# Optimization experiments

Measured on AMD Instinct MI355X. Metric: run time of the kernel, lower is better.

The kernel has to match this reference:

```python
import jax, jax.numpy as jnp
import numpy as np

N_NODES = 100000
F_IN = 128
F_HID = 64  # gcn_filters = [64, 64]
MLP_HID = 128


def setup_inputs() -> dict:
    key = jax.random.key(0)
    ks = jax.random.split(key, 12)
    E, Q = 3200000, 1000000
    feature = jax.random.normal(ks[0], (N_NODES, F_IN), dtype=jnp.float32)
    edges = jax.random.randint(ks[1], (2, E), 0, N_NODES, dtype=jnp.int32)
    i = jax.random.randint(ks[2], (Q,), 0, N_NODES, dtype=jnp.int32)
    j = jax.random.randint(ks[3], (Q,), 0, N_NODES, dtype=jnp.int32)
    s = lambda d: 1.0 / jnp.sqrt(d)
    W1 = jax.random.normal(ks[4], (F_IN, F_HID), dtype=jnp.float32) * s(F_IN)
    b1 = jnp.zeros((F_HID,), dtype=jnp.float32)
    W2 = jax.random.normal(ks[5], (F_HID, F_HID), dtype=jnp.float32) * s(F_HID)
    b2 = jnp.zeros((F_HID,), dtype=jnp.float32)
    fc1_W = jax.random.normal(ks[6], (2 * F_HID, MLP_HID), dtype=jnp.float32) * s(2 * F_HID)
    fc1_b = jnp.zeros((MLP_HID,), dtype=jnp.float32)
    fc2_W = jax.random.normal(ks[7], (MLP_HID, 2), dtype=jnp.float32) * s(MLP_HID)
    fc2_b = jnp.zeros((2,), dtype=jnp.float32)
    return {"feature": feature, "edges": edges, "i": i, "j": j,
            "W1": W1, "b1": b1, "W2": W2, "b2": b2,
            "fc1_W": fc1_W, "fc1_b": fc1_b, "fc2_W": fc2_W, "fc2_b": fc2_b}


def _gcn_layer(x, W, b, src, dst, norm, n):
    h = x @ W
    msg = h[src] * norm[:, None]
    return jax.ops.segment_sum(msg, dst, num_segments=n) + b


def reference(feature, edges, i, j, W1, b1, W2, b2, fc1_W, fc1_b, fc2_W, fc2_b):
    n = feature.shape[0]
    loops = jnp.arange(n, dtype=edges.dtype)
    src = jnp.concatenate([edges[0], loops])
    dst = jnp.concatenate([edges[1], loops])
    deg = jax.ops.segment_sum(jnp.ones(src.shape[0], feature.dtype), dst, num_segments=n)
    dinv = jax.lax.rsqrt(jnp.maximum(deg, 1e-12))
    norm = dinv[src] * dinv[dst]
    h = jax.nn.relu(_gcn_layer(feature, W1, b1, src, dst, norm, n))
    out = _gcn_layer(h, W2, b2, src, dst, norm, n)  # [N, F_HID]
    embd = jnp.concatenate([out[i], out[j]], axis=-1)  # [Q, 2*F_HID]
    hid = jax.nn.relu(embd @ fc1_W + fc1_b)
    return hid @ fc2_W + fc2_b
```

## Files before the change

### kernel.cpp

```cpp
#include <hip/hip_runtime.h>
#include <hip/hip_bf16.h>
#include <hip/hip_fp16.h>
#include <cstdint>

#define F_IN 128
#define F_HID 64
#define NB 64
#define MAXB 2048
#define NWG 256
#define PREPB 16
#define STAGE 12800

typedef _Float16 half8 __attribute__((ext_vector_type(8)));
typedef float floatx4 __attribute__((ext_vector_type(4)));

__device__ __forceinline__ float bf2f(unsigned short u) {
  return __uint_as_float(((unsigned int)u) << 16);
}
__device__ __forceinline__ unsigned short f2bf(float f) {
  unsigned int u = __float_as_uint(f);
  u += 0x7FFFu + ((u >> 16) & 1u);
  return (unsigned short)(u >> 16);
}
__device__ __forceinline__ float h2f(unsigned short u) {
  return __half2float(__ushort_as_half(u));
}
__device__ __forceinline__ unsigned short f2h(float f) {
  return __half_as_ushort(__float2half(f));
}

__global__ __launch_bounds__(64) void k_detect(const unsigned int* __restrict__ Xw,
                                               int* __restrict__ flag) {
  int lane = threadIdx.x;
  int cnt = 0;
  for (int t = lane; t < 256; t += 64) {
    unsigned int ex = (Xw[t] >> 7) & 0xFFu;
    cnt += (ex >= 117u && ex <= 137u) ? 1 : 0;
  }
#pragma unroll
  for (int off = 32; off > 0; off >>= 1) cnt += __shfl_xor(cnt, off, 64);
  if (lane == 0) *flag = (cnt >= 128) ? 1 : 0;
}

__global__ __launch_bounds__(256) void k_front(const void* __restrict__ Xv,
                                               unsigned short* __restrict__ Xh, int total8,
                                               const void* __restrict__ W1v,
                                               const void* __restrict__ W2v,
                                               const void* __restrict__ fc1Wv,
                                               unsigned short* __restrict__ fW1,
                                               unsigned short* __restrict__ fW2,
                                               unsigned short* __restrict__ fPR,
                                               const int* __restrict__ dst,
                                               int* __restrict__ hist, int E, int B, int chunk,
                                               const int* __restrict__ flagp) {
  __shared__ int lh[MAXB];
  const int bid = blockIdx.x;
  if (bid < NWG) {
    int w = bid, tid = threadIdx.x;
    for (int b = tid; b < B; b += 256) lh[b] = 0;
    __syncthreads();
    int e0 = w * chunk, e1 = min(E, e0 + chunk);
    for (int e = e0 + tid; e < e1; e += 256) atomicAdd(&lh[dst[e] >> 6], 1);
    __syncthreads();
    for (int b = tid; b < B; b += 256) hist[w * B + b] = lh[b];
    return;
  }
  const bool isb = (*flagp != 0);
  if (bid < NWG + PREPB) {
    int tid = (bid - NWG) * 256 + threadIdx.x;
    int stride = PREPB * 256;
    for (int e = tid; e < F_IN * F_HID; e += stride) {
      int k = e >> 6, n = e & 63;
      unsigned short v = isb ? f2h(bf2f(((const unsigned short*)W1v)[e]))
                             : f2h(((const float*)W1v)[e]);
      int c = k >> 5, q = (k >> 3) & 3, j = k & 7, t = n >> 4, m = n & 15;
      fW1[((c * 4 + t) * 64 + q * 16 + m) * 8 + j] = v;
    }
    for (int e = tid; e < F_HID * F_HID; e += stride) {
      int k = e >> 6, n = e & 63;
      unsigned short v = isb ? f2h(bf2f(((const unsigned short*)W2v)[e]))
                             : f2h(((const float*)W2v)[e]);
      int c = k >> 5, q = (k >> 3) & 3, j = k & 7, t = n >> 4, m = n & 15;
      fW2[((c * 4 + t) * 64 + q * 16 + m) * 8 + j] = v;
    }
    for (int ge = tid; ge < 4 * F_HID * 64; ge += stride) {
      int g = ge >> 12, e = ge & 4095;
      int k = e >> 6, n = e & 63;
      int src = (((g & 2) ? 64 : 0) + k) * 128 + (g & 1) * 64 + n;
      unsigned short v = isb ? f2h(bf2f(((const unsigned short*)fc1Wv)[src]))
                             : f2h(((const float*)fc1Wv)[src]);
      int c = k >> 5, q = (k >> 3) & 3, j = k & 7, t = n >> 4, m = n & 15;
      fPR[g * 4096 + ((c * 4 + t) * 64 + q * 16 + m) * 8 + j] = v;
    }
    return;
  }
  int t = (bid - (NWG + PREPB)) * 256 + threadIdx.x;
  int stride = (gridDim.x - (NWG + PREPB)) * 256;
  for (; t < total8; t += stride) {
    unsigned short r[8];
    if (isb) {
      uint4 d = reinterpret_cast<const uint4*>(Xv)[t];
      r[0] = f2h(__uint_as_float(d.x << 16));
      r[1] = f2h(__uint_as_float(d.x & 0xFFFF0000u));
      r[2] = f2h(__uint_as_float(d.y << 16));
      r[3] = f2h(__uint_as_float(d.y & 0xFFFF0000u));
      r[4] = f2h(__uint_as_float(d.z << 16));
      r[5] = f2h(__uint_as_float(d.z & 0xFFFF0000u));
      r[6] = f2h(__uint_as_float(d.w << 16));
      r[7] = f2h(__uint_as_float(d.w & 0xFFFF0000u));
    } else {
      float4 a = reinterpret_cast<const float4*>(Xv)[2 * t];
      float4 b = reinterpret_cast<const float4*>(Xv)[2 * t + 1];
      r[0] = f2h(a.x); r[1] = f2h(a.y); r[2] = f2h(a.z); r[3] = f2h(a.w);
      r[4] = f2h(b.x); r[5] = f2h(b.y); r[6] = f2h(b.z); r[7] = f2h(b.w);
    }
    uint4 o;
    o.x = (unsigned int)r[0] | ((unsigned int)r[1] << 16);
    o.y = (unsigned int)r[2] | ((unsigned int)r[3] << 16);
    o.z = (unsigned int)r[4] | ((unsigned int)r[5] << 16);
    o.w = (unsigned int)r[6] | ((unsigned int)r[7] << 16);
    reinterpret_cast<uint4*>(Xh)[t] = o;
  }
}

__global__ __launch_bounds__(256) void k_bscan1(int* __restrict__ hist,
                                                int* __restrict__ btot, int B) {
  const int WPL = NWG / 64;
  int b = (blockIdx.x * 256 + threadIdx.x) >> 6;
  int lane = threadIdx.x & 63;
  if (b >= B) return;
  int v[WPL];
  int s = 0;
#pragma unroll
  for (int k = 0; k < WPL; k++) {
    v[k] = hist[(size_t)(lane * WPL + k) * B + b];
    s += v[k];
  }
  int pre = s;
#pragma unroll
  for (int off = 1; off < 64; off <<= 1) {
    int t = __shfl_up(pre, off, 64);
    if (lane >= off) pre += t;
  }
  int running = pre - s;
#pragma unroll
  for (int k = 0; k < WPL; k++) {
    int val = v[k];
    hist[(size_t)(lane * WPL + k) * B + b] = running;
    running += val;
  }
  if (lane == 63) btot[b] = running;
}

__global__ __launch_bounds__(256) void k_bscan2(const int* __restrict__ btot,
                                                int* __restrict__ boff, int B, int E) {
  __shared__ int partial[256];
  int t = threadIdx.x;
  int CH = (B + 255) / 256;
  int b0 = t * CH, b1 = min(B, b0 + CH);
  int tt = 0;
  for (int b = b0; b < b1; b++) tt += btot[b];
  partial[t] = tt;
  __syncthreads();
  if (t == 0) {
    int acc = 0;
    for (int i = 0; i < 256; i++) { int v = partial[i]; partial[i] = acc; acc += v; }
  }
  __syncthreads();
  int off = partial[t];
  for (int b = b0; b < b1; b++) { boff[b] = off; off += btot[b]; }
  if (t == 255) boff[B] = E;
}

__global__ __launch_bounds__(256) void k_bfill(const int* __restrict__ src,
                                               const int* __restrict__ dst,
                                               const int* __restrict__ hist,
                                               const int* __restrict__ boff,
                                               int* __restrict__ buck,
                                               int E, int B, int chunk) {
  __shared__ int gcur[MAXB];
  __shared__ int lexcl[MAXB];
  __shared__ int lcur[MAXB];
  __shared__ int stage[STAGE];
  __shared__ unsigned short bdex[STAGE];
  __shared__ int part[256];
  const int w = blockIdx.x, tid = threadIdx.x;
  for (int b = tid; b < B; b += 256) gcur[b] = boff[b] + hist[w * B + b];
  int e0 = w * chunk, e1 = min(E, e0 + chunk);
  for (int s0 = e0; s0 < e1; s0 += STAGE) {
    int s1 = min(e1, s0 + STAGE);
    int cnt = s1 - s0;
    for (int b = tid; b < B; b += 256) lexcl[b] = 0;
    __syncthreads();
    for (int e = s0 + tid; e < s1; e += 256) atomicAdd(&lexcl[dst[e] >> 6], 1);
    __syncthreads();
    int CH = (B + 255) >> 8;
    int b0 = tid * CH, b1 = min(B, b0 + CH);
    int s = 0;
    for (int b = b0; b < b1; b++) s += lexcl[b];
    part[tid] = s;
    __syncthreads();
    if (tid == 0) {
      int acc = 0;
      for (int i = 0; i < 256; i++) { int v = part[i]; part[i] = acc; acc += v; }
    }
    __syncthreads();
    int run = part[tid];
    for (int b = b0; b < b1; b++) {
      int v = lexcl[b];
      lexcl[b] = run;
      lcur[b] = run;
      run += v;
    }
    __syncthreads();
    for (int e = s0 + tid; e < s1; e += 256) {
      int d = dst[e];
      int b = d >> 6;
      int p = atomicAdd(&lcur[b], 1);
      stage[p] = ((d & 63) << 17) | src[e];
      bdex[p] = (unsigned short)b;
    }
    __syncthreads();
    for (int p = tid; p < cnt; p += 256) {
      int b = bdex[p];
      buck[gcur[b] + (p - lexcl[b])] = stage[p];
    }
    __syncthreads();
    for (int b = tid; b < B; b += 256) gcur[b] += lcur[b] - lexcl[b];
    __syncthreads();
  }
}

__global__ __launch_bounds__(256) void k_bsort(const int* __restrict__ buck,
                                               const int* __restrict__ boff,
                                               int* __restrict__ csr,
                                               int* __restrict__ noff,
                                               float* __restrict__ dinv, int N) {
  __shared__ int bin[NB][4];
  __shared__ int excl[NB];
  int b = blockIdx.x, tid = threadIdx.x;
  const int rep = tid & 3;
  for (int i = tid; i < NB * 4; i += 256) ((int*)bin)[i] = 0;
  __syncthreads();
  int r0 = boff[b], r1 = boff[b + 1];
  for (int r = r0 + tid; r < r1; r += 256) atomicAdd(&bin[buck[r] >> 17][rep], 1);
  __syncthreads();
  if (tid < NB)
    excl[tid] = bin[tid][0] + bin[tid][1] + bin[tid][2] + bin[tid][3];
  __syncthreads();
  if (tid == 0) {
    int acc = 0;
    for (int i = 0; i < NB; i++) { int v = excl[i]; excl[i] = acc; acc += v; }
  }
  __syncthreads();
  if (tid < NB) {
    int n = b * NB + tid;
    int c0 = bin[tid][0], c1 = bin[tid][1], c2 = bin[tid][2], c3 = bin[tid][3];
    if (n < N) {
      dinv[n] = rsqrtf((float)(c0 + c1 + c2 + c3) + 1.0f);
      noff[n] = r0 + excl[tid];
    }
    int base = excl[tid];
    bin[tid][0] = base;
    bin[tid][1] = base + c0;
    bin[tid][2] = base + c0 + c1;
    bin[tid][3] = base + c0 + c1 + c2;
  }
  if (b == gridDim.x - 1 && tid == 128) noff[N] = r1;
  __syncthreads();
  for (int r = r0 + tid; r < r1; r += 256) {
    int rec = buck[r];
    int p = atomicAdd(&bin[rec >> 17][rep], 1);
    csr[r0 + p] = rec & 0x1FFFF;
  }
}


__global__ __launch_bounds__(256, 4) void k_gemm1(const unsigned short* __restrict__ Xh,
                                                  const unsigned short* __restrict__ fW1,
                                                  const float* __restrict__ dinv,
                                                  unsigned short* __restrict__ G, int N) {
  int tid = threadIdx.x;
  const int lane = tid & 63, wave = tid >> 6;
  const int m = lane & 15, q = lane >> 4;
  half8 bfrag[4][4];
#pragma unroll
  for (int c = 0; c < 4; c++)
#pragma unroll
    for (int t = 0; t < 4; t++)
      bfrag[c][t] = *reinterpret_cast<const half8*>(fW1 + ((c * 4 + t) * 64 + lane) * 8);
  int ntiles = (N + 15) >> 4;
  for (int tile = blockIdx.x * 4 + wave; tile < ntiles; tile += gridDim.x * 4) {
    int r0 = tile << 4;
    int rm = r0 + m; rm = rm < N ? rm : N - 1;
    floatx4 acc[4] = {{0.f,0.f,0.f,0.f},{0.f,0.f,0.f,0.f},{0.f,0.f,0.f,0.f},{0.f,0.f,0.f,0.f}};
#pragma unroll
    for (int c = 0; c < 4; c++) {
      half8 a = *reinterpret_cast<const half8*>(Xh + (size_t)rm * F_IN + c * 32 + q * 8);
#pragma unroll
      for (int t = 0; t < 4; t++)
        acc[t] = __builtin_amdgcn_mfma_f32_16x16x32_f16(a, bfrag[c][t], acc[t], 0, 0, 0);
    }
#pragma unroll
    for (int rr = 0; rr < 4; rr++) {
      int grow = r0 + q * 4 + rr;
      if (grow < N) {
        float dv = dinv[grow];
#pragma unroll
        for (int t = 0; t < 4; t++)
          G[(size_t)grow * F_HID + t * 16 + m] = f2h(acc[t][rr] * dv);
      }
    }
  }
}

__global__ __launch_bounds__(256, 4) void k_gemm2(const unsigned short* __restrict__ O,
                                                  const unsigned short* __restrict__ fW2,
                                                  const float* __restrict__ dinv,
                                                  unsigned short* __restrict__ G, int N) {
  int tid = threadIdx.x;
  const int lane = tid & 63, wave = tid >> 6;
  const int m = lane & 15, q = lane >> 4;
  half8 bfrag[2][4];
#pragma unroll
  for (int c = 0; c < 2; c++)
#pragma unroll
    for (int t = 0; t < 4; t++)
      bfrag[c][t] = *reinterpret_cast<const half8*>(fW2 + ((c * 4 + t) * 64 + lane) * 8);
  int ntiles = (N + 15) >> 4;
  for (int tile = blockIdx.x * 4 + wave; tile < ntiles; tile += gridDim.x * 4) {
    int r0 = tile << 4;
    int rm = r0 + m; rm = rm < N ? rm : N - 1;
    floatx4 acc[4] = {{0.f,0.f,0.f,0.f},{0.f,0.f,0.f,0.f},{0.f,0.f,0.f,0.f},{0.f,0.f,0.f,0.f}};
#pragma unroll
    for (int c = 0; c < 2; c++) {
      half8 a = *reinterpret_cast<const half8*>(O + (size_t)rm * F_HID + c * 32 + q * 8);
#pragma unroll
      for (int t = 0; t < 4; t++)
        acc[t] = __builtin_amdgcn_mfma_f32_16x16x32_f16(a, bfrag[c][t], acc[t], 0, 0, 0);
    }
#pragma unroll
    for (int rr = 0; rr < 4; rr++) {
      int grow = r0 + q * 4 + rr;
      if (grow < N) {
        float dv = dinv[grow];
#pragma unroll
        for (int t = 0; t < 4; t++)
          G[(size_t)grow * F_HID + t * 16 + m] = f2h(acc[t][rr] * dv);
      }
    }
  }
}

template <bool RELU>
__global__ __launch_bounds__(256) void k_agg(const int* __restrict__ csr,
                                             const int* __restrict__ noff,
                                             const unsigned short* __restrict__ H,
                                             const float* __restrict__ dinv,
                                             const void* __restrict__ bias,
                                             unsigned short* __restrict__ OUT, int N,
                                             const int* __restrict__ flagp) {
  const bool isb = (*flagp != 0);
  const int lane = threadIdx.x & 63;
  const int g = lane >> 4, l16 = lane & 15;
  const int gw = (blockIdx.x * 256 + threadIdx.x) >> 6;
  const int nW = (gridDim.x * 256) >> 6;
  float bv[4];
#pragma unroll
  for (int d = 0; d < 4; d++)
    bv[d] = isb ? bf2f(((const unsigned short*)bias)[l16 * 4 + d])
                : ((const float*)bias)[l16 * 4 + d];
  for (int n = gw; n < N; n += nW) {
    int start = noff[n], end = noff[n + 1];
    float a0 = 0.f, a1 = 0.f, a2 = 0.f, a3 = 0.f;
    for (int e0 = start; e0 < end; e0 += 64) {
      int ee = e0 + lane;
      int idx = (ee < end) ? csr[ee] : 0;
      int m = end - e0; m = m < 64 ? m : 64;
      int nc = m >> 2;
      int c = 0;
      for (; c + 8 <= nc; c += 8) {
        int s[8];
#pragma unroll
        for (int u = 0; u < 8; u++) s[u] = __shfl(idx, (c + u) * 4 + g, 64);
        ushort4 v[8];
#pragma unroll
        for (int u = 0; u < 8; u++)
          v[u] = *reinterpret_cast<const ushort4*>(H + (size_t)s[u] * F_HID + l16 * 4);
#pragma unroll
        for (int u = 0; u < 8; u++) {
          a0 += h2f(v[u].x); a1 += h2f(v[u].y);
          a2 += h2f(v[u].z); a3 += h2f(v[u].w);
        }
      }
      for (; c < nc; c++) {
        int s0 = __shfl(idx, c * 4 + g, 64);
        ushort4 v0 = *reinterpret_cast<const ushort4*>(H + (size_t)s0 * F_HID + l16 * 4);
        a0 += h2f(v0.x); a1 += h2f(v0.y); a2 += h2f(v0.z); a3 += h2f(v0.w);
      }
      int rem = m & 3;
      if (rem) {
        int s0 = __shfl(idx, nc * 4 + g, 64);
        if (g < rem) {
          ushort4 v0 = *reinterpret_cast<const ushort4*>(H + (size_t)s0 * F_HID + l16 * 4);
          a0 += h2f(v0.x); a1 += h2f(v0.y); a2 += h2f(v0.z); a3 += h2f(v0.w);
        }
      }
    }
    a0 += __shfl_xor(a0, 16, 64); a0 += __shfl_xor(a0, 32, 64);
    a1 += __shfl_xor(a1, 16, 64); a1 += __shfl_xor(a1, 32, 64);
    a2 += __shfl_xor(a2, 16, 64); a2 += __shfl_xor(a2, 32, 64);
    a3 += __shfl_xor(a3, 16, 64); a3 += __shfl_xor(a3, 32, 64);
    ushort4 sv = *reinterpret_cast<const ushort4*>(H + (size_t)n * F_HID + l16 * 4);
    float dv = dinv[n];
    float o0 = (a0 + h2f(sv.x)) * dv + bv[0];
    float o1 = (a1 + h2f(sv.y)) * dv + bv[1];
    float o2 = (a2 + h2f(sv.z)) * dv + bv[2];
    float o3 = (a3 + h2f(sv.w)) * dv + bv[3];
    if (RELU) {
      o0 = fmaxf(o0, 0.f); o1 = fmaxf(o1, 0.f);
      o2 = fmaxf(o2, 0.f); o3 = fmaxf(o3, 0.f);
    }
    if (lane < 16) {
      ushort4 ov;
      ov.x = f2h(o0); ov.y = f2h(o1); ov.z = f2h(o2); ov.w = f2h(o3);
      *reinterpret_cast<ushort4*>(OUT + (size_t)n * F_HID + l16 * 4) = ov;
    }
  }
}

__global__ __launch_bounds__(512) void k_query(const unsigned short* __restrict__ O,
                                               const unsigned short* __restrict__ fPR,
                                               const int* __restrict__ qi,
                                               const int* __restrict__ qj,
                                               const void* __restrict__ fc1b,
                                               const void* __restrict__ fc2W,
                                               const void* __restrict__ fc2b,
                                               void* __restrict__ out, int Q,
                                               const int* __restrict__ flagp) {
  __shared__ unsigned short sB[4 * 4096];
  const bool isb = (*flagp != 0);
  int tid = threadIdx.x;
  {
    const uint4* srcp = reinterpret_cast<const uint4*>(fPR);
    uint4* dstp = reinterpret_cast<uint4*>(sB);
#pragma unroll
    for (int r = 0; r < 4; r++) dstp[tid + r * 512] = srcp[tid + r * 512];
  }
  const int lane = tid & 63, wave = tid >> 6;
  const int m_ = lane & 15, qk = lane >> 4;
  float bb[8], w0[8], w1[8];
#pragma unroll
  for (int T = 0; T < 8; T++) {
    int h = T * 16 + m_;
    if (isb) {
      bb[T] = bf2f(((const unsigned short*)fc1b)[h]);
      w0[T] = bf2f(((const unsigned short*)fc2W)[h * 2 + 0]);
      w1[T] = bf2f(((const unsigned short*)fc2W)[h * 2 + 1]);
    } else {
      bb[T] = ((const float*)fc1b)[h];
      w0[T] = ((const float*)fc2W)[h * 2 + 0];
      w1[T] = ((const float*)fc2W)[h * 2 + 1];
    }
  }
  float ob0 = isb ? bf2f(((const unsigned short*)fc2b)[0]) : ((const float*)fc2b)[0];
  float ob1 = isb ? bf2f(((const unsigned short*)fc2b)[1]) : ((const float*)fc2b)[1];
  __syncthreads();
  const half8* sBv = reinterpret_cast<const half8*>(sB);

  const int ntiles = (Q + 15) >> 4;
  const int nW = gridDim.x * 8;
  int tile = blockIdx.x * 8 + wave;
  if (tile >= ntiles) return;

  auto ldidx = [&](int t, int& iq, int& jq) {
    if (t < ntiles) {
      int q = t * 16 + m_;
      int qq = q < Q ? q : Q - 1;
      iq = qi[qq];
      jq = qj[qq];
    }
  };
  auto gather = [&](int iq, int jq, half8& I0, half8& I1, half8& J0, half8& J1) {
    const half8* pI = reinterpret_cast<const half8*>(O + (size_t)iq * F_HID) + qk;
    const half8* pJ = reinterpret_cast<const half8*>(O + (size_t)jq * F_HID) + qk;
    I0 = pI[0]; I1 = pI[4];
    J0 = pJ[0]; J1 = pJ[4];
  };

  int iqn = 0, jqn = 0;
  ldidx(tile, iqn, jqn);
  half8 I0, I1, J0, J1;
  gather(iqn, jqn, I0, I1, J0, J1);
  ldidx(tile + nW, iqn, jqn);

  for (; tile < ntiles; tile += nW) {
    half8 nI0, nI1, nJ0, nJ1;
    gather(iqn, jqn, nI0, nI1, nJ0, nJ1);
    ldidx(tile + 2 * nW, iqn, jqn);

    float r0[4] = {0.f, 0.f, 0.f, 0.f};
    float r1[4] = {0.f, 0.f, 0.f, 0.f};
    const floatx4 zz = {0.f, 0.f, 0.f, 0.f};
#pragma unroll
    for (int h = 0; h < 2; h++) {
      floatx4 acc[4];
#pragma unroll
      for (int tt = 0; tt < 4; tt++) acc[tt] = zz;
      __builtin_amdgcn_s_setprio(1);
#pragma unroll
      for (int tt = 0; tt < 4; tt++) {
        acc[tt] = __builtin_amdgcn_mfma_f32_16x16x32_f16(
            I0, sBv[h * 512 + tt * 64 + lane], acc[tt], 0, 0, 0);
        acc[tt] = __builtin_amdgcn_mfma_f32_16x16x32_f16(
            I1, sBv[h * 512 + (4 + tt) * 64 + lane], acc[tt], 0, 0, 0);
        acc[tt] = __builtin_amdgcn_mfma_f32_16x16x32_f16(
            J0, sBv[(2 + h) * 512 + tt * 64 + lane], acc[tt], 0, 0, 0);
        acc[tt] = __builtin_amdgcn_mfma_f32_16x16x32_f16(
            J1, sBv[(2 + h) * 512 + (4 + tt) * 64 + lane], acc[tt], 0, 0, 0);
      }
      __builtin_amdgcn_s_setprio(0);
#pragma unroll
      for (int tt = 0; tt < 4; tt++) {
        int T = h * 4 + tt;
#pragma unroll
        for (int rr = 0; rr < 4; rr++) {
          float hv = fmaxf(acc[tt][rr] + bb[T], 0.f);
          r0[rr] += hv * w0[T];
          r1[rr] += hv * w1[T];
        }
      }
      __builtin_amdgcn_sched_barrier(0);
    }
#pragma unroll
    for (int rr = 0; rr < 4; rr++) {
      float a0 = r0[rr], a1 = r1[rr];
#pragma unroll
      for (int off = 8; off > 0; off >>= 1) {
        a0 += __shfl_xor(a0, off, 16);
        a1 += __shfl_xor(a1, off, 16);
      }
      if (m_ == 0) {
        int q = tile * 16 + qk * 4 + rr;
        if (q < Q) {
          if (isb) {
            *reinterpret_cast<ushort2*>((unsigned short*)out + (size_t)q * 2) =
                make_ushort2(f2bf(a0 + ob0), f2bf(a1 + ob1));
          } else {
            *reinterpret_cast<float2*>((float*)out + (size_t)q * 2) =
                make_float2(a0 + ob0, a1 + ob1);
          }
        }
      }
    }
    I0 = nI0; I1 = nI1; J0 = nJ0; J1 = nJ1;
  }
}

extern "C" void kernel_launch(void* const* d_in, const int* in_sizes, int n_in,
                              void* d_out, int out_size, void* d_ws, size_t ws_size,
                              hipStream_t stream) {
  const void* X    = d_in[0];
  const int*  edges= (const int*)d_in[1];
  const int*  qi   = (const int*)d_in[2];
  const int*  qj   = (const int*)d_in[3];
  const void* W1   = d_in[4];
  const void* b1   = d_in[5];
  const void* W2   = d_in[6];
  const void* b2   = d_in[7];
  const void* fc1W = d_in[8];
  const void* fc1b = d_in[9];
  const void* fc2W = d_in[10];
  const void* fc2b = d_in[11];

  const int N = in_sizes[0] / F_IN;
  const int E = in_sizes[1] / 2;
  const int Q = in_sizes[2];
  const int B = (N + NB - 1) / NB;
  const int chunk = (E + NWG - 1) / NWG;

  char* ws = (char*)d_ws;
  size_t off = 0;
  auto alloc = [&](size_t bytes) -> void* {
    void* p = ws + off;
    off += (bytes + 255) & ~(size_t)255;
    return p;
  };
  int*            flag = (int*)alloc(4);
  float*          dinv = (float*)alloc((size_t)N * 4);
  unsigned short* Xh   = (unsigned short*)alloc((size_t)N * F_IN * 2);
  unsigned short* G    = (unsigned short*)alloc((size_t)N * F_HID * 2);
  unsigned short* O    = (unsigned short*)alloc((size_t)N * F_HID * 2);
  unsigned short* fW1  = (unsigned short*)alloc((size_t)F_IN * F_HID * 2);
  unsigned short* fW2  = (unsigned short*)alloc((size_t)F_HID * F_HID * 2);
  unsigned short* fPR  = (unsigned short*)alloc((size_t)4 * F_HID * 64 * 2);
  int* hist = (int*)alloc((size_t)NWG * B * 4);
  int* btot = (int*)alloc((size_t)(B + 1) * 4);
  int* boff = (int*)alloc((size_t)(B + 1) * 4);
  int* buck = (int*)alloc((size_t)E * 4);
  int* csr  = (int*)alloc((size_t)E * 4);
  int* noff = (int*)alloc((size_t)(N + 1) * 4);
  (void)ws_size; (void)n_in; (void)out_size;

  const int* esrc = edges;
  const int* edst = edges + E;

  k_detect<<<1, 64, 0, stream>>>((const unsigned int*)X, flag);
  k_front<<<2048, 256, 0, stream>>>(X, Xh, N * F_IN / 8, W1, W2, fc1W, fW1, fW2, fPR,
                                    edst, hist, E, B, chunk, flag);

  k_bscan1<<<(B + 3) / 4, 256, 0, stream>>>(hist, btot, B);
  k_bscan2<<<1, 256, 0, stream>>>(btot, boff, B, E);
  k_bfill<<<NWG, 256, 0, stream>>>(esrc, edst, hist, boff, buck, E, B, chunk);
  k_bsort<<<B, 256, 0, stream>>>(buck, boff, csr, noff, dinv, N);

  k_gemm1<<<2048, 256, 0, stream>>>(Xh, fW1, dinv, G, N);
  k_agg<true><<<2048, 256, 0, stream>>>(csr, noff, G, dinv, b1, O, N, flag);

  k_gemm2<<<2048, 256, 0, stream>>>(O, fW2, dinv, G, N);
  k_agg<false><<<2048, 256, 0, stream>>>(csr, noff, G, dinv, b2, O, N, flag);

  k_query<<<1024, 512, 0, stream>>>(O, fPR, qi, qj, fc1b, fc2W, fc2b, d_out, Q, flag);
}
```

Baseline: 438.3 us.

## Remove detect and bscan2 launches by inlining dtype detection and offset scan

Drops the separate dtype-detect kernel: each consuming kernel now scans the first 256 input words itself to decide bf16 vs fp32. Folds the single-block bucket-offset scan into k_bfill, where every block recomputes the exclusive scan of btot and block 0 writes boff. Also widens the k_bsort per-bin atomic replication from 4 to 8 to reduce shared-atomic contention. Together these remove two serial launches at the cost of redundant per-thread and per-block work.

```diff
diff --git a/kernel.cpp b/kernel.cpp
--- a/kernel.cpp
+++ b/kernel.cpp
@@ -29,17 +29,15 @@
   return __half_as_ushort(__float2half(f));
 }
 
-__global__ __launch_bounds__(64) void k_detect(const unsigned int* __restrict__ Xw,
-                                               int* __restrict__ flag) {
-  int lane = threadIdx.x;
+__device__ __forceinline__ bool detect_bf16(const void* Xv) {
+  const unsigned int* Xw = (const unsigned int*)Xv;
   int cnt = 0;
-  for (int t = lane; t < 256; t += 64) {
+#pragma unroll 8
+  for (int t = 0; t < 256; t++) {
     unsigned int ex = (Xw[t] >> 7) & 0xFFu;
     cnt += (ex >= 117u && ex <= 137u) ? 1 : 0;
   }
-#pragma unroll
-  for (int off = 32; off > 0; off >>= 1) cnt += __shfl_xor(cnt, off, 64);
-  if (lane == 0) *flag = (cnt >= 128) ? 1 : 0;
+  return cnt >= 128;
 }
 
 __global__ __launch_bounds__(256) void k_front(const void* __restrict__ Xv,
@@ -51,8 +49,7 @@
                                                unsigned short* __restrict__ fW2,
                                                unsigned short* __restrict__ fPR,
                                                const int* __restrict__ dst,
-                                               int* __restrict__ hist, int E, int B, int chunk,
-                                               const int* __restrict__ flagp) {
+                                               int* __restrict__ hist, int E, int B, int chunk) {
   __shared__ int lh[MAXB];
   const int bid = blockIdx.x;
   if (bid < NWG) {
@@ -65,7 +62,7 @@
     for (int b = tid; b < B; b += 256) hist[w * B + b] = lh[b];
     return;
   }
-  const bool isb = (*flagp != 0);
+  const bool isb = detect_bf16(Xv);
   if (bid < NWG + PREPB) {
     int tid = (bid - NWG) * 256 + threadIdx.x;
     int stride = PREPB * 256;
@@ -152,30 +149,11 @@
   if (lane == 63) btot[b] = running;
 }
 
-__global__ __launch_bounds__(256) void k_bscan2(const int* __restrict__ btot,
-                                                int* __restrict__ boff, int B, int E) {
-  __shared__ int partial[256];
-  int t = threadIdx.x;
-  int CH = (B + 255) / 256;
-  int b0 = t * CH, b1 = min(B, b0 + CH);
-  int tt = 0;
-  for (int b = b0; b < b1; b++) tt += btot[b];
-  partial[t] = tt;
-  __syncthreads();
-  if (t == 0) {
-    int acc = 0;
-    for (int i = 0; i < 256; i++) { int v = partial[i]; partial[i] = acc; acc += v; }
-  }
-  __syncthreads();
-  int off = partial[t];
-  for (int b = b0; b < b1; b++) { boff[b] = off; off += btot[b]; }
-  if (t == 255) boff[B] = E;
-}
-
 __global__ __launch_bounds__(256) void k_bfill(const int* __restrict__ src,
                                                const int* __restrict__ dst,
                                                const int* __restrict__ hist,
-                                               const int* __restrict__ boff,
+                                               const int* __restrict__ btot,
+                                               int* __restrict__ boff,
                                                int* __restrict__ buck,
                                                int E, int B, int chunk) {
   __shared__ int gcur[MAXB];
@@ -185,7 +163,28 @@
   __shared__ unsigned short bdex[STAGE];
   __shared__ int part[256];
   const int w = blockIdx.x, tid = threadIdx.x;
-  for (int b = tid; b < B; b += 256) gcur[b] = boff[b] + hist[w * B + b];
+  {
+    int CH = (B + 255) >> 8;
+    int b0 = tid * CH, b1 = min(B, b0 + CH);
+    int s = 0;
+    for (int b = b0; b < b1; b++) s += btot[b];
+    part[tid] = s;
+    __syncthreads();
+    if (tid == 0) {
+      int acc = 0;
+      for (int i = 0; i < 256; i++) { int v = part[i]; part[i] = acc; acc += v; }
+    }
+    __syncthreads();
+    int run = part[tid];
+    for (int b = b0; b < b1; b++) { lexcl[b] = run; run += btot[b]; }
+    __syncthreads();
+    for (int b = tid; b < B; b += 256) gcur[b] = lexcl[b] + hist[w * B + b];
+    if (w == 0) {
+      for (int b = tid; b < B; b += 256) boff[b] = lexcl[b];
+      if (tid == 0) boff[B] = E;
+    }
+    __syncthreads();
+  }
   int e0 = w * chunk, e1 = min(E, e0 + chunk);
   for (int s0 = e0; s0 < e1; s0 += STAGE) {
     int s1 = min(e1, s0 + STAGE);
@@ -236,17 +235,21 @@
                                                int* __restrict__ csr,
                                                int* __restrict__ noff,
                                                float* __restrict__ dinv, int N) {
-  __shared__ int bin[NB][4];
+  __shared__ int bin[NB][8];
   __shared__ int excl[NB];
   int b = blockIdx.x, tid = threadIdx.x;
-  const int rep = tid & 3;
-  for (int i = tid; i < NB * 4; i += 256) ((int*)bin)[i] = 0;
+  const int rep = tid & 7;
+  for (int i = tid; i < NB * 8; i += 256) ((int*)bin)[i] = 0;
   __syncthreads();
   int r0 = boff[b], r1 = boff[b + 1];
   for (int r = r0 + tid; r < r1; r += 256) atomicAdd(&bin[buck[r] >> 17][rep], 1);
   __syncthreads();
-  if (tid < NB)
-    excl[tid] = bin[tid][0] + bin[tid][1] + bin[tid][2] + bin[tid][3];
+  if (tid < NB) {
+    int t = 0;
+#pragma unroll
+    for (int r = 0; r < 8; r++) t += bin[tid][r];
+    excl[tid] = t;
+  }
   __syncthreads();
   if (tid == 0) {
     int acc = 0;
@@ -255,16 +258,16 @@
   __syncthreads();
   if (tid < NB) {
     int n = b * NB + tid;
-    int c0 = bin[tid][0], c1 = bin[tid][1], c2 = bin[tid][2], c3 = bin[tid][3];
+    int tot = 0;
+#pragma unroll
+    for (int r = 0; r < 8; r++) tot += bin[tid][r];
     if (n < N) {
-      dinv[n] = rsqrtf((float)(c0 + c1 + c2 + c3) + 1.0f);
+      dinv[n] = rsqrtf((float)tot + 1.0f);
       noff[n] = r0 + excl[tid];
     }
-    int base = excl[tid];
-    bin[tid][0] = base;
-    bin[tid][1] = base + c0;
-    bin[tid][2] = base + c0 + c1;
-    bin[tid][3] = base + c0 + c1 + c2;
+    int acc = excl[tid];
+#pragma unroll
+    for (int r = 0; r < 8; r++) { int c = bin[tid][r]; bin[tid][r] = acc; acc += c; }
   }
   if (b == gridDim.x - 1 && tid == 128) noff[N] = r1;
   __syncthreads();
@@ -359,8 +362,8 @@
                                              const float* __restrict__ dinv,
                                              const void* __restrict__ bias,
                                              unsigned short* __restrict__ OUT, int N,
-                                             const int* __restrict__ flagp) {
-  const bool isb = (*flagp != 0);
+                                             const void* __restrict__ Xv) {
+  const bool isb = detect_bf16(Xv);
   const int lane = threadIdx.x & 63;
   const int g = lane >> 4, l16 = lane & 15;
   const int gw = (blockIdx.x * 256 + threadIdx.x) >> 6;
@@ -437,9 +440,9 @@
                                                const void* __restrict__ fc2W,
                                                const void* __restrict__ fc2b,
                                                void* __restrict__ out, int Q,
-                                               const int* __restrict__ flagp) {
+                                               const void* __restrict__ Xv) {
   __shared__ unsigned short sB[4 * 4096];
-  const bool isb = (*flagp != 0);
+  const bool isb = detect_bf16(Xv);
   int tid = threadIdx.x;
   {
     const uint4* srcp = reinterpret_cast<const uint4*>(fPR);
@@ -586,7 +589,6 @@
     off += (bytes + 255) & ~(size_t)255;
     return p;
   };
-  int*            flag = (int*)alloc(4);
   float*          dinv = (float*)alloc((size_t)N * 4);
   unsigned short* Xh   = (unsigned short*)alloc((size_t)N * F_IN * 2);
   unsigned short* G    = (unsigned short*)alloc((size_t)N * F_HID * 2);
@@ -605,20 +607,18 @@
   const int* esrc = edges;
   const int* edst = edges + E;
 
-  k_detect<<<1, 64, 0, stream>>>((const unsigned int*)X, flag);
   k_front<<<2048, 256, 0, stream>>>(X, Xh, N * F_IN / 8, W1, W2, fc1W, fW1, fW2, fPR,
-                                    edst, hist, E, B, chunk, flag);
+                                    edst, hist, E, B, chunk);
 
   k_bscan1<<<(B + 3) / 4, 256, 0, stream>>>(hist, btot, B);
-  k_bscan2<<<1, 256, 0, stream>>>(btot, boff, B, E);
-  k_bfill<<<NWG, 256, 0, stream>>>(esrc, edst, hist, boff, buck, E, B, chunk);
+  k_bfill<<<NWG, 256, 0, stream>>>(esrc, edst, hist, btot, boff, buck, E, B, chunk);
   k_bsort<<<B, 256, 0, stream>>>(buck, boff, csr, noff, dinv, N);
 
   k_gemm1<<<2048, 256, 0, stream>>>(Xh, fW1, dinv, G, N);
-  k_agg<true><<<2048, 256, 0, stream>>>(csr, noff, G, dinv, b1, O, N, flag);
+  k_agg<true><<<2048, 256, 0, stream>>>(csr, noff, G, dinv, b1, O, N, X);
 
   k_gemm2<<<2048, 256, 0, stream>>>(O, fW2, dinv, G, N);
-  k_agg<false><<<2048, 256, 0, stream>>>(csr, noff, G, dinv, b2, O, N, flag);
-
-  k_query<<<1024, 512, 0, stream>>>(O, fPR, qi, qj, fc1b, fc2W, fc2b, d_out, Q, flag);
-}
+  k_agg<false><<<2048, 256, 0, stream>>>(csr, noff, G, dinv, b2, O, N, X);
+
+  k_query<<<1024, 512, 0, stream>>>(O, fPR, qi, qj, fc1b, fc2W, fc2b, d_out, Q, X);
+}
```

Measured after the change: 465.7 us. 6.3% more time.
